# Kernel optimization log

Hardware: AMD Instinct MI355X
Metric: run time of the kernel (lower is better)

## Reference

```python
import jax, jax.numpy as jnp
import numpy as np

EMBED_DIM = 1024
PROJ_DIM = 64
B, S = 8, 2048


def setup_inputs() -> dict:
    key = jax.random.key(0)
    k1, k2, k3 = jax.random.split(key, 3)
    context = jax.random.normal(k1, (S, B, EMBED_DIM), dtype=jnp.float32)
    prior = jax.random.uniform(k2, (B, S), dtype=jnp.float32)
    # xavier_uniform for (2*proj_dim, embed_dim)
    bound = float(np.sqrt(6.0 / (2 * PROJ_DIM + EMBED_DIM)))
    proj_weight = jax.random.uniform(k3, (2 * PROJ_DIM, EMBED_DIM), dtype=jnp.float32,
                                     minval=-bound, maxval=bound)
    proj_bias = jnp.zeros((2 * PROJ_DIM,), dtype=jnp.float32)
    return {"context": context, "prior": prior,
            "proj_weight": proj_weight, "proj_bias": proj_bias}


def reference(context, prior, proj_weight, proj_bias):
    # context: (S, B, E) -> (B, S, E)
    x = jnp.transpose(context, (1, 0, 2))
    b, s, e = x.shape
    qk = jnp.einsum('bse,pe->bsp', x, proj_weight) + proj_bias  # (B,S,2P)
    query, key = jnp.split(qk, 2, axis=2)
    # neighbor scores, scaled by embed_dim (as in the original)
    fwd = jnp.sum(query[:, :-1] * key[:, 1:], axis=-1) / e   # (B,S-1) score i<->i+1
    bwd = jnp.sum(query[:, 1:] * key[:, :-1], axis=-1) / e   # (B,S-1) score i<->i-1
    ninf = jnp.full((b, 1), -jnp.inf, dtype=x.dtype)
    score = jnp.stack([jnp.concatenate([fwd, ninf], axis=1),
                       jnp.concatenate([ninf, bwd], axis=1)], axis=-1)  # (B,S,2)
    prob = jax.nn.softmax(score, axis=-1)
    # torch .roll(shifts=-1) with no dims flattens the whole tensor: reproduce that
    shift_prob = jnp.roll(prob[:, :, 1].reshape(-1), -1).reshape(b, s)
    prob0 = jnp.sqrt(prob[:, :, 0] * shift_prob + 1e-6)      # (B,S)
    neighbor_attn = prior + (1.0 - prior) * prob0
    log_prob = jnp.log(neighbor_attn)
    # Original places log_prob[:, :-1] on the superdiagonal and hits it with
    # triu matmuls on both sides: C[i,j] = sum_{m=i}^{j-1} log_prob[m] for j>i.
    # Equivalent O(n^2): prefix sums cs[t] = sum_{m<t} log_prob[m].
    cs = jnp.concatenate([jnp.zeros((b, 1), dtype=x.dtype),
                          jnp.cumsum(log_prob[:, :-1], axis=1)], axis=1)  # (B,S)
    D = cs[:, None, :] - cs[:, :, None]            # D[b,i,j] = cs[j]-cs[i]
    i_idx = jnp.arange(s)
    upper = i_idx[None, :] > i_idx[:, None]        # (S,S) j>i
    M = jnp.where(upper[None], D, -D)              # C + C^T (symmetric)
    constituent_attn = jnp.exp(M)
    diag = i_idx[None, :] == i_idx[:, None]
    constituent_attn = jnp.where(diag[None], jnp.zeros((), x.dtype), constituent_attn)
    return constituent_attn, neighbor_attn
```

## Files before the change

### kernel.cpp

```cpp
#include <hip/hip_runtime.h>
#include <cstdint>
#include <cstddef>

#define E_DIM 1024
#define PD 64
#define NP 128
#define B_DIM 8
#define S_DIM 2048
#define M_TOT (B_DIM * S_DIM)

#define BMR 32
#define BK 32
#define NCH (E_DIM / BK)

typedef __attribute__((ext_vector_type(8))) short short8v;
typedef __attribute__((ext_vector_type(4))) float f32x4;

__device__ __forceinline__ void cvt_hilo(const f32x4 v0, const f32x4 v1,
                                         short8v& h, short8v& l) {
    const unsigned MSK = 0xFFFF0000u;
    unsigned a0 = __float_as_uint(v0.x), a1 = __float_as_uint(v0.y);
    unsigned a2 = __float_as_uint(v0.z), a3 = __float_as_uint(v0.w);
    unsigned a4 = __float_as_uint(v1.x), a5 = __float_as_uint(v1.y);
    unsigned a6 = __float_as_uint(v1.z), a7 = __float_as_uint(v1.w);
    float l0 = v0.x - __uint_as_float(a0 & MSK);
    float l1 = v0.y - __uint_as_float(a1 & MSK);
    float l2 = v0.z - __uint_as_float(a2 & MSK);
    float l3 = v0.w - __uint_as_float(a3 & MSK);
    float l4 = v1.x - __uint_as_float(a4 & MSK);
    float l5 = v1.y - __uint_as_float(a5 & MSK);
    float l6 = v1.z - __uint_as_float(a6 & MSK);
    float l7 = v1.w - __uint_as_float(a7 & MSK);
    union { unsigned u[4]; short8v s; } H, L;
    H.u[0] = (a1 & MSK) | (a0 >> 16);
    H.u[1] = (a3 & MSK) | (a2 >> 16);
    H.u[2] = (a5 & MSK) | (a4 >> 16);
    H.u[3] = (a7 & MSK) | (a6 >> 16);
    L.u[0] = (__float_as_uint(l1) & MSK) | (__float_as_uint(l0) >> 16);
    L.u[1] = (__float_as_uint(l3) & MSK) | (__float_as_uint(l2) >> 16);
    L.u[2] = (__float_as_uint(l5) & MSK) | (__float_as_uint(l4) >> 16);
    L.u[3] = (__float_as_uint(l7) & MSK) | (__float_as_uint(l6) >> 16);
    h = H.s; l = L.s;
}

__global__ __launch_bounds__(256) void conv_w(const float* __restrict__ W,
                                              ushort* __restrict__ hiImg,
                                              ushort* __restrict__ loImg) {
    const int t = blockIdx.x * 256 + threadIdx.x;
    const int c  = t & 127;
    const int q  = (t >> 7) & 3;
    const int ch = t >> 9;
    const float* src = W + (size_t)c * E_DIM + ch * 32 + q * 8;
    const f32x4 v0 = *(const f32x4*)src;
    const f32x4 v1 = *(const f32x4*)(src + 4);
    short8v h, l;
    cvt_hilo(v0, v1, h, l);
    const size_t off = ((size_t)(ch * 4 + q) * NP + c) * 8;
    *(short8v*)&hiImg[off] = h;
    *(short8v*)&loImg[off] = l;
}

__global__ __launch_bounds__(256, 2) void gemm_qk(const float* __restrict__ A,
                                                  const ushort* __restrict__ hiImg,
                                                  const ushort* __restrict__ loImg,
                                                  const float* __restrict__ bias,
                                                  float* __restrict__ qk) {
    __shared__ __align__(16) float As[2][BMR][BK];
    const int tid = threadIdx.x;
    const int m0  = blockIdx.x * BMR;
    const int w   = tid >> 6;
    const int ln  = tid & 63;
    const int lr  = ln >> 3;
    const int g8  = ln & 7;
    const int row16 = ln & 15;
    const int kq    = ln >> 4;
    const int r7    = row16 & 7;
    const int sg0 = ((((kq << 1) | 0) ^ r7) & 7) << 2;
    const int sg1 = ((((kq << 1) | 1) ^ r7) & 7) << 2;

    const float* aS = A + (size_t)(m0 + w * 8 + lr) * E_DIM + (g8 << 2);
    float* const aDst0 = &As[0][0][0] + (w * 8 + lr) * BK + ((g8 ^ lr) << 2);
    float* const aDst1 = &As[1][0][0] + (w * 8 + lr) * BK + ((g8 ^ lr) << 2);
    const ushort* hS = hiImg + ((size_t)kq * NP + w * 32 + row16) * 8;
    const ushort* lS = loImg + ((size_t)kq * NP + w * 32 + row16) * 8;

    float bias2[2];
    bias2[0] = bias[w * 32 + row16];
    bias2[1] = bias[w * 32 + 16 + row16];

    f32x4 acc[2][2];
#pragma unroll
    for (int i = 0; i < 2; ++i)
#pragma unroll
        for (int j = 0; j < 2; ++j) acc[i][j] = (f32x4){0.f, 0.f, 0.f, 0.f};

    f32x4 aP0, aP1;
    short8v wh00, wh01, wl00, wl01;
    short8v wh10, wh11, wl10, wl11;

    aP0 = *(const f32x4*)(aS);
    aP1 = *(const f32x4*)(aS + BK);
    wh00 = *(const short8v*)(hS);
    wh01 = *(const short8v*)(hS + 128);
    wl00 = *(const short8v*)(lS);
    wl01 = *(const short8v*)(lS + 128);
    wh10 = *(const short8v*)(hS + 4096);
    wh11 = *(const short8v*)(hS + 4096 + 128);
    wl10 = *(const short8v*)(lS + 4096);
    wl11 = *(const short8v*)(lS + 4096 + 128);
    *(f32x4*)aDst0 = aP0;
    asm volatile("s_waitcnt lgkmcnt(0)" ::: "memory");
    __builtin_amdgcn_sched_barrier(0);

#define GBODY(P, CH, APcur, APother, WH0, WH1, WL0, WL1, DSTother, SRCbuf)          \
    {                                                                               \
        __builtin_amdgcn_s_barrier();                                               \
        __builtin_amdgcn_sched_barrier(0);                                          \
        if ((CH) + 1 < NCH) { *(f32x4*)(DSTother) = APother; }                      \
        if ((CH) + 2 < NCH) {                                                       \
            APcur = *(const f32x4*)(aS + ((CH) + 2) * BK);                          \
        }                                                                           \
        short8v ah0, al0, ah1, al1;                                                 \
        {                                                                           \
            const float* b0 = &As[SRCbuf][row16][0];                                \
            cvt_hilo(*(const f32x4*)(b0 + sg0), *(const f32x4*)(b0 + sg1), ah0, al0); \
            const float* b1 = &As[SRCbuf][16 + row16][0];                           \
            cvt_hilo(*(const f32x4*)(b1 + sg0), *(const f32x4*)(b1 + sg1), ah1, al1); \
        }                                                                           \
        acc[0][0] = __builtin_amdgcn_mfma_f32_16x16x32_bf16(ah0, WH0, acc[0][0], 0, 0, 0); \
        acc[0][0] = __builtin_amdgcn_mfma_f32_16x16x32_bf16(ah0, WL0, acc[0][0], 0, 0, 0); \
        acc[0][0] = __builtin_amdgcn_mfma_f32_16x16x32_bf16(al0, WH0, acc[0][0], 0, 0, 0); \
        acc[0][1] = __builtin_amdgcn_mfma_f32_16x16x32_bf16(ah0, WH1, acc[0][1], 0, 0, 0); \
        acc[0][1] = __builtin_amdgcn_mfma_f32_16x16x32_bf16(ah0, WL1, acc[0][1], 0, 0, 0); \
        acc[0][1] = __builtin_amdgcn_mfma_f32_16x16x32_bf16(al0, WH1, acc[0][1], 0, 0, 0); \
        acc[1][0] = __builtin_amdgcn_mfma_f32_16x16x32_bf16(ah1, WH0, acc[1][0], 0, 0, 0); \
        acc[1][0] = __builtin_amdgcn_mfma_f32_16x16x32_bf16(ah1, WL0, acc[1][0], 0, 0, 0); \
        acc[1][0] = __builtin_amdgcn_mfma_f32_16x16x32_bf16(al1, WH0, acc[1][0], 0, 0, 0); \
        acc[1][1] = __builtin_amdgcn_mfma_f32_16x16x32_bf16(ah1, WH1, acc[1][1], 0, 0, 0); \
        acc[1][1] = __builtin_amdgcn_mfma_f32_16x16x32_bf16(ah1, WL1, acc[1][1], 0, 0, 0); \
        acc[1][1] = __builtin_amdgcn_mfma_f32_16x16x32_bf16(al1, WH1, acc[1][1], 0, 0, 0); \
        if ((CH) + 2 < NCH) {                                                       \
            WH0 = *(const short8v*)(hS + (size_t)((CH) + 2) * 4096);                \
            WH1 = *(const short8v*)(hS + (size_t)((CH) + 2) * 4096 + 128);          \
            WL0 = *(const short8v*)(lS + (size_t)((CH) + 2) * 4096);                \
            WL1 = *(const short8v*)(lS + (size_t)((CH) + 2) * 4096 + 128);          \
        }                                                                           \
        asm volatile("s_waitcnt lgkmcnt(0)" ::: "memory");                          \
        __builtin_amdgcn_sched_barrier(0);                                          \
    }

#pragma unroll 1
    for (int c2 = 0; c2 < NCH / 2; ++c2) {
        const int ch0 = 2 * c2;
        GBODY(0, ch0, aP0, aP1, wh00, wh01, wl00, wl01, aDst1, 0)
        const int ch1 = 2 * c2 + 1;
        GBODY(1, ch1, aP1, aP0, wh10, wh11, wl10, wl11, aDst0, 1)
    }
#undef GBODY

#pragma unroll
    for (int fi = 0; fi < 2; ++fi)
#pragma unroll
        for (int fj = 0; fj < 2; ++fj) {
#pragma unroll
            for (int r = 0; r < 4; ++r) {
                const int m = m0 + fi * 16 + kq * 4 + r;
                const int p = w * 32 + fj * 16 + row16;
                qk[(size_t)m * NP + p] = acc[fi][fj][r] + bias2[fj];
            }
        }
}

__global__ __launch_bounds__(256) void neighbor_probs(const float* __restrict__ qk,
                                                      float* __restrict__ p0,
                                                      float* __restrict__ p1) {
    const int m = blockIdx.x * 4 + (threadIdx.x >> 6);
    const int lane = threadIdx.x & 63;
    const int s = m >> 3;
    const int b = m & 7;

    const float q = qk[(size_t)m * NP + lane];
    const float kn = (s < S_DIM - 1) ? qk[(size_t)(m + B_DIM) * NP + PD + lane] : 0.f;
    const float kp = (s > 0) ? qk[(size_t)(m - B_DIM) * NP + PD + lane] : 0.f;
    float f = q * kn;
    float g = q * kp;
#pragma unroll
    for (int off = 32; off; off >>= 1) {
        f += __shfl_xor(f, off);
        g += __shfl_xor(g, off);
    }
    if (lane == 0) {
        const float s0 = f * (1.f / (float)E_DIM);
        const float s1 = g * (1.f / (float)E_DIM);
        float P0, P1;
        if (s == S_DIM - 1) { P0 = 0.f; P1 = 1.f; }
        else if (s == 0)    { P0 = 1.f; P1 = 0.f; }
        else {
            const float mx = fmaxf(s0, s1);
            const float e0 = __expf(s0 - mx), e1 = __expf(s1 - mx);
            const float inv = 1.f / (e0 + e1);
            P0 = e0 * inv; P1 = e1 * inv;
        }
        p0[b * S_DIM + s] = P0;
        p1[b * S_DIM + s] = P1;
    }
}

__global__ __launch_bounds__(256) void combine_scan(const float* __restrict__ p0,
                                                    const float* __restrict__ p1,
                                                    const float* __restrict__ prior,
                                                    float* __restrict__ out_na,
                                                    float* __restrict__ cs) {
    const int b = blockIdx.x;
    const int tid = threadIdx.x;
    __shared__ float sh[256];

    const int base = b * S_DIM + tid * 8;
    float incl[8];
    float run = 0.f;
#pragma unroll
    for (int u = 0; u < 8; ++u) {
        const int fidx = base + u;
        int nf = fidx + 1;
        if (nf == B_DIM * S_DIM) nf = 0;
        const float P0 = p0[fidx];
        const float sp = p1[nf];
        const float pr = prior[fidx];
        const float na = pr + (1.f - pr) * sqrtf(P0 * sp + 1e-6f);
        out_na[fidx] = na;
        run += __logf(na);
        incl[u] = run;
    }
    sh[tid] = run;
    __syncthreads();
    for (int off = 1; off < 256; off <<= 1) {
        float v = sh[tid];
        if (tid >= off) v += sh[tid - off];
        __syncthreads();
        sh[tid] = v;
        __syncthreads();
    }
    const float offset = (tid > 0) ? sh[tid - 1] : 0.f;
#pragma unroll
    for (int u = 0; u < 8; ++u) {
        cs[base + u] = offset + ((u > 0) ? incl[u - 1] : 0.f);
    }
}

__global__ __launch_bounds__(256) void big_out(const float* __restrict__ cs,
                                               float* __restrict__ out) {
    const int bi = blockIdx.x;
    const int b = bi >> 11;
    const int i = bi & (S_DIM - 1);
    const float ci = cs[b * S_DIM + i];
    const float* crow = cs + (size_t)b * S_DIM;
    float* orow = out + (size_t)bi * S_DIM;
    const int j0 = threadIdx.x * 8;
#pragma unroll
    for (int h = 0; h < 2; ++h) {
        const int j = j0 + h * 4;
        const f32x4 cj = *(const f32x4*)&crow[j];
        f32x4 o;
        {
            const int jj = j + 0; const float m = (jj > i) ? (cj.x - ci) : (ci - cj.x);
            o.x = (jj == i) ? 0.f : __expf(m);
        }
        {
            const int jj = j + 1; const float m = (jj > i) ? (cj.y - ci) : (ci - cj.y);
            o.y = (jj == i) ? 0.f : __expf(m);
        }
        {
            const int jj = j + 2; const float m = (jj > i) ? (cj.z - ci) : (ci - cj.z);
            o.z = (jj == i) ? 0.f : __expf(m);
        }
        {
            const int jj = j + 3; const float m = (jj > i) ? (cj.w - ci) : (ci - cj.w);
            o.w = (jj == i) ? 0.f : __expf(m);
        }
        *(f32x4*)&orow[j] = o;
    }
}

extern "C" void kernel_launch(void* const* d_in, const int* in_sizes, int n_in,
                              void* d_out, int out_size, void* d_ws, size_t ws_size,
                              hipStream_t stream) {
    const float* context = (const float*)d_in[0];
    const float* prior   = (const float*)d_in[1];
    const float* W       = (const float*)d_in[2];
    const float* bias    = (const float*)d_in[3];
    float* out = (float*)d_out;

    float* qk = (float*)d_ws;
    float* p0 = qk + (size_t)M_TOT * NP;
    float* p1 = p0 + M_TOT;
    float* cs = p1 + M_TOT;
    ushort* hiImg = (ushort*)out;
    ushort* loImg = hiImg + (size_t)NP * E_DIM;
    float* na_out = out + (size_t)B_DIM * S_DIM * S_DIM;

    conv_w<<<64, 256, 0, stream>>>(W, hiImg, loImg);
    gemm_qk<<<M_TOT / BMR, 256, 0, stream>>>(context, hiImg, loImg, bias, qk);
    neighbor_probs<<<M_TOT / 4, 256, 0, stream>>>(qk, p0, p1);
    combine_scan<<<B_DIM, 256, 0, stream>>>(p0, p1, prior, na_out, cs);
    big_out<<<M_TOT, 256, 0, stream>>>(cs, out);
}
```

Baseline: 66.23 us.

## Split K across two wave groups in GEMM with direct global-to-LDS loads

The qk projection GEMM now launches 512 threads per block, with two groups of four waves each handling half of the K dimension. The partial accumulators are reduced through a shared-memory buffer before the bias is added and the result stored. Activation tiles are loaded with global_load_lds instead of being staged through registers, and the hand-placed waitcnt and scheduling barriers are replaced with __syncthreads. This aims to increase memory-level parallelism and latency hiding, at the cost of an extra LDS reduction and reliance on correct waiting for the asynchronous LDS loads.

```diff
diff --git a/kernel.cpp b/kernel.cpp
--- a/kernel.cpp
+++ b/kernel.cpp
@@ -11,10 +11,17 @@
 
 #define BMR 32
 #define BK 32
-#define NCH (E_DIM / BK)
+#define NCHH 16
 
 typedef __attribute__((ext_vector_type(8))) short short8v;
 typedef __attribute__((ext_vector_type(4))) float f32x4;
+
+__device__ __forceinline__ void gload16(const void* g, void* l) {
+    __builtin_amdgcn_global_load_lds(
+        (const __attribute__((address_space(1))) unsigned int*)g,
+        (__attribute__((address_space(3))) unsigned int*)(uintptr_t)l,
+        16, 0, 0);
+}
 
 __device__ __forceinline__ void cvt_hilo(const f32x4 v0, const f32x4 v1,
                                          short8v& h, short8v& l) {
@@ -60,15 +67,18 @@
     *(short8v*)&loImg[off] = l;
 }
 
-__global__ __launch_bounds__(256, 2) void gemm_qk(const float* __restrict__ A,
+__global__ __launch_bounds__(512, 4) void gemm_qk(const float* __restrict__ A,
                                                   const ushort* __restrict__ hiImg,
                                                   const ushort* __restrict__ loImg,
                                                   const float* __restrict__ bias,
                                                   float* __restrict__ qk) {
-    __shared__ __align__(16) float As[2][BMR][BK];
+    __shared__ __align__(16) float As[2][2][BMR][BK];
+    __shared__ __align__(16) float Cred[BMR][NP];
     const int tid = threadIdx.x;
     const int m0  = blockIdx.x * BMR;
     const int w   = tid >> 6;
+    const int h   = w >> 2;
+    const int wv  = w & 3;
     const int ln  = tid & 63;
     const int lr  = ln >> 3;
     const int g8  = ln & 7;
@@ -78,15 +88,17 @@
     const int sg0 = ((((kq << 1) | 0) ^ r7) & 7) << 2;
     const int sg1 = ((((kq << 1) | 1) ^ r7) & 7) << 2;
 
-    const float* aS = A + (size_t)(m0 + w * 8 + lr) * E_DIM + (g8 << 2);
-    float* const aDst0 = &As[0][0][0] + (w * 8 + lr) * BK + ((g8 ^ lr) << 2);
-    float* const aDst1 = &As[1][0][0] + (w * 8 + lr) * BK + ((g8 ^ lr) << 2);
-    const ushort* hS = hiImg + ((size_t)kq * NP + w * 32 + row16) * 8;
-    const ushort* lS = loImg + ((size_t)kq * NP + w * 32 + row16) * 8;
+    const int srow = wv * 8 + lr;
+    const float* aS = A + (size_t)(m0 + srow) * E_DIM + h * (NCHH * BK)
+                        + ((g8 ^ (srow & 7)) << 2);
+    const ushort* hS = hiImg + (size_t)(h * NCHH) * 4096
+                             + ((size_t)kq * NP + wv * 32 + row16) * 8;
+    const ushort* lS = loImg + (size_t)(h * NCHH) * 4096
+                             + ((size_t)kq * NP + wv * 32 + row16) * 8;
 
     float bias2[2];
-    bias2[0] = bias[w * 32 + row16];
-    bias2[1] = bias[w * 32 + 16 + row16];
+    bias2[0] = bias[wv * 32 + row16];
+    bias2[1] = bias[wv * 32 + 16 + row16];
 
     f32x4 acc[2][2];
 #pragma unroll
@@ -94,37 +106,31 @@
 #pragma unroll
         for (int j = 0; j < 2; ++j) acc[i][j] = (f32x4){0.f, 0.f, 0.f, 0.f};
 
-    f32x4 aP0, aP1;
-    short8v wh00, wh01, wl00, wl01;
-    short8v wh10, wh11, wl10, wl11;
-
-    aP0 = *(const f32x4*)(aS);
-    aP1 = *(const f32x4*)(aS + BK);
-    wh00 = *(const short8v*)(hS);
-    wh01 = *(const short8v*)(hS + 128);
-    wl00 = *(const short8v*)(lS);
-    wl01 = *(const short8v*)(lS + 128);
-    wh10 = *(const short8v*)(hS + 4096);
-    wh11 = *(const short8v*)(hS + 4096 + 128);
-    wl10 = *(const short8v*)(lS + 4096);
-    wl11 = *(const short8v*)(lS + 4096 + 128);
-    *(f32x4*)aDst0 = aP0;
-    asm volatile("s_waitcnt lgkmcnt(0)" ::: "memory");
-    __builtin_amdgcn_sched_barrier(0);
-
-#define GBODY(P, CH, APcur, APother, WH0, WH1, WL0, WL1, DSTother, SRCbuf)          \
+    short8v whA0, whA1, wlA0, wlA1;
+    short8v whB0, whB1, wlB0, wlB1;
+
+    gload16(aS, &As[h][0][wv * 8][0]);
+    whA0 = *(const short8v*)(hS);
+    whA1 = *(const short8v*)(hS + 128);
+    wlA0 = *(const short8v*)(lS);
+    wlA1 = *(const short8v*)(lS + 128);
+
+#define GBODY(CH, WH0, WH1, WL0, WL1, NWH0, NWH1, NWL0, NWL1)                       \
     {                                                                               \
-        __builtin_amdgcn_s_barrier();                                               \
-        __builtin_amdgcn_sched_barrier(0);                                          \
-        if ((CH) + 1 < NCH) { *(f32x4*)(DSTother) = APother; }                      \
-        if ((CH) + 2 < NCH) {                                                       \
-            APcur = *(const f32x4*)(aS + ((CH) + 2) * BK);                          \
+        const int buf = (CH) & 1;                                                   \
+        __syncthreads();                    \
+        if ((CH) + 1 < NCHH) {                                                      \
+            gload16(aS + ((CH) + 1) * BK, &As[h][buf ^ 1][wv * 8][0]);              \
+            NWH0 = *(const short8v*)(hS + (size_t)((CH) + 1) * 4096);               \
+            NWH1 = *(const short8v*)(hS + (size_t)((CH) + 1) * 4096 + 128);         \
+            NWL0 = *(const short8v*)(lS + (size_t)((CH) + 1) * 4096);               \
+            NWL1 = *(const short8v*)(lS + (size_t)((CH) + 1) * 4096 + 128);         \
         }                                                                           \
         short8v ah0, al0, ah1, al1;                                                 \
         {                                                                           \
-            const float* b0 = &As[SRCbuf][row16][0];                                \
+            const float* b0 = &As[h][buf][row16][0];                                \
             cvt_hilo(*(const f32x4*)(b0 + sg0), *(const f32x4*)(b0 + sg1), ah0, al0); \
-            const float* b1 = &As[SRCbuf][16 + row16][0];                           \
+            const float* b1 = &As[h][buf][16 + row16][0];                           \
             cvt_hilo(*(const f32x4*)(b1 + sg0), *(const f32x4*)(b1 + sg1), ah1, al1); \
         }                                                                           \
         acc[0][0] = __builtin_amdgcn_mfma_f32_16x16x32_bf16(ah0, WH0, acc[0][0], 0, 0, 0); \
@@ -139,36 +145,39 @@
         acc[1][1] = __builtin_amdgcn_mfma_f32_16x16x32_bf16(ah1, WH1, acc[1][1], 0, 0, 0); \
         acc[1][1] = __builtin_amdgcn_mfma_f32_16x16x32_bf16(ah1, WL1, acc[1][1], 0, 0, 0); \
         acc[1][1] = __builtin_amdgcn_mfma_f32_16x16x32_bf16(al1, WH1, acc[1][1], 0, 0, 0); \
-        if ((CH) + 2 < NCH) {                                                       \
-            WH0 = *(const short8v*)(hS + (size_t)((CH) + 2) * 4096);                \
-            WH1 = *(const short8v*)(hS + (size_t)((CH) + 2) * 4096 + 128);          \
-            WL0 = *(const short8v*)(lS + (size_t)((CH) + 2) * 4096);                \
-            WL1 = *(const short8v*)(lS + (size_t)((CH) + 2) * 4096 + 128);          \
-        }                                                                           \
-        asm volatile("s_waitcnt lgkmcnt(0)" ::: "memory");                          \
-        __builtin_amdgcn_sched_barrier(0);                                          \
     }
 
 #pragma unroll 1
-    for (int c2 = 0; c2 < NCH / 2; ++c2) {
-        const int ch0 = 2 * c2;
-        GBODY(0, ch0, aP0, aP1, wh00, wh01, wl00, wl01, aDst1, 0)
-        const int ch1 = 2 * c2 + 1;
-        GBODY(1, ch1, aP1, aP0, wh10, wh11, wl10, wl11, aDst0, 1)
+    for (int c2 = 0; c2 < NCHH / 2; ++c2) {
+        GBODY(2 * c2,     whA0, whA1, wlA0, wlA1, whB0, whB1, wlB0, wlB1)
+        GBODY(2 * c2 + 1, whB0, whB1, wlB0, wlB1, whA0, whA1, wlA0, wlA1)
     }
 #undef GBODY
 
-#pragma unroll
-    for (int fi = 0; fi < 2; ++fi)
-#pragma unroll
-        for (int fj = 0; fj < 2; ++fj) {
-#pragma unroll
-            for (int r = 0; r < 4; ++r) {
-                const int m = m0 + fi * 16 + kq * 4 + r;
-                const int p = w * 32 + fj * 16 + row16;
-                qk[(size_t)m * NP + p] = acc[fi][fj][r] + bias2[fj];
+    if (h == 1) {
+#pragma unroll
+        for (int fi = 0; fi < 2; ++fi)
+#pragma unroll
+            for (int fj = 0; fj < 2; ++fj)
+#pragma unroll
+                for (int r = 0; r < 4; ++r)
+                    Cred[fi * 16 + kq * 4 + r][wv * 32 + fj * 16 + row16] = acc[fi][fj][r];
+    }
+    __syncthreads();
+    if (h == 0) {
+#pragma unroll
+        for (int fi = 0; fi < 2; ++fi)
+#pragma unroll
+            for (int fj = 0; fj < 2; ++fj) {
+#pragma unroll
+                for (int r = 0; r < 4; ++r) {
+                    const int mr = fi * 16 + kq * 4 + r;
+                    const int p  = wv * 32 + fj * 16 + row16;
+                    qk[(size_t)(m0 + mr) * NP + p] =
+                        acc[fi][fj][r] + Cred[mr][p] + bias2[fj];
+                }
             }
-        }
+    }
 }
 
 __global__ __launch_bounds__(256) void neighbor_probs(const float* __restrict__ qk,
@@ -299,7 +308,7 @@
     float* na_out = out + (size_t)B_DIM * S_DIM * S_DIM;
 
     conv_w<<<64, 256, 0, stream>>>(W, hiImg, loImg);
-    gemm_qk<<<M_TOT / BMR, 256, 0, stream>>>(context, hiImg, loImg, bias, qk);
+    gemm_qk<<<M_TOT / BMR, 512, 0, stream>>>(context, hiImg, loImg, bias, qk);
     neighbor_probs<<<M_TOT / 4, 256, 0, stream>>>(qk, p0, p1);
     combine_scan<<<B_DIM, 256, 0, stream>>>(p0, p1, prior, na_out, cs);
     big_out<<<M_TOT, 256, 0, stream>>>(cs, out);
```

Measured after the change: 64.04 us. -3.3%, faster.
